# Performance work log

Measured on AMD Instinct MI355X. Metric: run time of the kernel, lower is better.

The kernel has to match this reference:

```python
import jax, jax.numpy as jnp
import numpy as np

N_NODE = 100000
N_EDGE = 1600000
D_FEAT = 64
DEPTH = 3
BASEALPHA = 1.0


def setup_inputs() -> dict:
    key = jax.random.key(0)
    k1, k2, k3 = jax.random.split(key, 3)
    x = jax.random.normal(k1, (N_NODE, D_FEAT), dtype=jnp.float32)
    edge_index = jax.random.randint(k2, (2, N_EDGE), 0, N_NODE, dtype=jnp.int64)
    edge_attr = jax.random.uniform(k3, (N_EDGE,), dtype=jnp.float32)
    # learnable polynomial coefficients, init = min(1/alpha, 1) = 1.0
    alphas = jnp.ones((DEPTH + 1,), dtype=jnp.float32)
    return {"x": x, "edge_index": edge_index, "edge_attr": edge_attr, "alphas": alphas}


def reference(x, edge_index, edge_attr, alphas):
    n = x.shape[0]
    row, col = edge_index[0], edge_index[1]
    # GCN symmetric degree normalization: val_e = d_row^-1/2 * w_e * d_col^-1/2
    deg = jax.ops.segment_sum(edge_attr, row, num_segments=n)
    safe_deg = jnp.where(deg > 0, deg, 1.0)
    dinv = jnp.where(deg > 0, jax.lax.rsqrt(safe_deg), 0.0)
    val = dinv[row] * edge_attr * dinv[col]  # [E]

    a = BASEALPHA * jnp.tanh(alphas)  # [depth+1]

    def spmm(h):  # (adj @ h): out[i] = sum_{e: row_e=i} val_e * h[col_e]
        return jax.ops.segment_sum(val[:, None] * h[col], row, num_segments=n)

    # PowerConv recurrence: x_0 = x; x_L = a_L * (adj @ x_{L-1})
    xs = [x]
    for L in range(1, DEPTH + 1):
        xs.append(a[L] * spmm(xs[-1]))
    return jnp.stack(xs, axis=1)  # [N, depth+1, d]
```

## Files before the change

kernel.cpp:

```cpp
#include <hip/hip_runtime.h>
#include <math.h>

#define N_NODE 100000
#define N_EDGE 1600000
#define D_FEAT 64
#define DEPTH  3
#define OUT_STRIDE ((DEPTH + 1) * D_FEAT)

#define NB  256
#define RPB 391
#define CAP 8192
#define S1_BS 512
#define S1_CHUNK 8192
#define S1_BLOCKS ((N_EDGE + S1_CHUNK - 1) / S1_CHUNK)

#define DEG_SCALE 33554432.0f

__device__ __forceinline__ unsigned int bf16_rne(float f) {
    unsigned int u = __float_as_uint(f);
    return (u + 0x7FFFu + ((u >> 16) & 1u)) >> 16;
}

__global__ __launch_bounds__(S1_BS) void stage1_bucket(
        const int* __restrict__ ei, const float* __restrict__ ea,
        int* __restrict__ bucket_cursor, int2* __restrict__ bucket) {
    __shared__ int hist[NB];
    __shared__ int segb[NB];
    int tid = threadIdx.x;
    int e0 = blockIdx.x * S1_CHUNK;

    for (int i = tid; i < NB; i += S1_BS) hist[i] = 0;
    __syncthreads();

    for (int k = 0; k < S1_CHUNK; k += S1_BS) {
        int e = e0 + k + tid;
        if (e < N_EDGE) {
            int r = ei[e];
            atomicAdd(&hist[r / RPB], 1);
        }
    }
    __syncthreads();

    for (int i = tid; i < NB; i += S1_BS) {
        int h = hist[i];
        segb[i] = (h > 0) ? atomicAdd(&bucket_cursor[i], h) : 0;
        hist[i] = 0;
    }
    __syncthreads();

    for (int k = 0; k < S1_CHUNK; k += S1_BS) {
        int e = e0 + k + tid;
        if (e < N_EDGE) {
            int r  = ei[e];
            int b  = r / RPB;
            int rl = r - b * RPB;
            int c  = ei[N_EDGE + e];
            float w = ea[e];
            int lofs = atomicAdd(&hist[b], 1);
            int pos  = segb[b] + lofs;
            if (pos < CAP)
                bucket[(size_t)b * CAP + pos] =
                    make_int2((rl << 17) | c, __float_as_int(w));
        }
    }
}

__global__ void bucket_scan_kernel(const int* __restrict__ bucket_cursor,
                                   int* __restrict__ bucket_base,
                                   const float* __restrict__ alphas,
                                   float* __restrict__ a_vals) {
    __shared__ int sc[NB];
    int tid = threadIdx.x;
    int v = bucket_cursor[tid];
    sc[tid] = v;
    __syncthreads();
    for (int off = 1; off < NB; off <<= 1) {
        int t = (tid >= off) ? sc[tid - off] : 0;
        __syncthreads();
        sc[tid] += t;
        __syncthreads();
    }
    bucket_base[tid] = sc[tid] - v;
    if (tid < DEPTH + 1) a_vals[tid] = tanhf(alphas[tid]);
}

__global__ __launch_bounds__(1024) void stage2a_rows(
        const int2* __restrict__ bucket, const int* __restrict__ bucket_cnt,
        const int* __restrict__ bucket_base,
        int* __restrict__ row_ptr, int* __restrict__ row_end,
        float* __restrict__ dinv) {
    __shared__ int          rcnt[RPB];
    __shared__ unsigned int wdeg[RPB];
    __shared__ int          sc[512];
    int b = blockIdx.x, tid = threadIdx.x;

    for (int i = tid; i < RPB; i += 1024) { rcnt[i] = 0; wdeg[i] = 0u; }
    __syncthreads();

    int cnt = bucket_cnt[b];
    const int2* src = bucket + (size_t)b * CAP;
    for (int i = tid; i < cnt; i += 1024) {
        int2 e = src[i];
        int rl = e.x >> 17;
        float w = __int_as_float(e.y);
        atomicAdd(&rcnt[rl], 1);
        atomicAdd(&wdeg[rl], (unsigned int)(w * DEG_SCALE + 0.5f));
    }
    __syncthreads();

    int v = 0;
    if (tid < 512) {
        v = (tid < RPB) ? rcnt[tid] : 0;
        sc[tid] = v;
    }
    __syncthreads();
    for (int off = 1; off < 512; off <<= 1) {
        int t = 0;
        if (tid < 512 && tid >= off) t = sc[tid - off];
        __syncthreads();
        if (tid < 512) sc[tid] += t;
        __syncthreads();
    }

    if (tid < RPB) {
        int row = b * RPB + tid;
        if (row < N_NODE) {
            int base = bucket_base[b] + sc[tid] - v;
            row_ptr[row] = base;
            row_end[row] = base + rcnt[tid];
            float d = (float)wdeg[tid] * (1.0f / DEG_SCALE);
            dinv[row] = (d > 0.0f) ? rsqrtf(d) : 0.0f;
        }
    }
}

__global__ __launch_bounds__(1024) void stage2b_place(
        const int2* __restrict__ bucket, const int* __restrict__ bucket_cnt,
        const int* __restrict__ bucket_base, const int* __restrict__ row_ptr,
        const float* __restrict__ dinv, int2* __restrict__ csr) {
    __shared__ int   lcur[RPB];
    __shared__ float dinv_l[RPB];
    __shared__ int2  staged[CAP];
    int b = blockIdx.x, tid = threadIdx.x;
    int base_b = bucket_base[b];
    int row0 = b * RPB;

    for (int i = tid; i < RPB; i += 1024) {
        int row = row0 + i;
        if (row < N_NODE) {
            lcur[i]   = row_ptr[row] - base_b;
            dinv_l[i] = dinv[row];
        } else {
            lcur[i] = 0; dinv_l[i] = 0.0f;
        }
    }
    __syncthreads();

    int cnt = bucket_cnt[b];
    const int2* src = bucket + (size_t)b * CAP;
    for (int i = tid; i < cnt; i += 1024) {
        int2 e = src[i];
        int rl = e.x >> 17;
        int c  = e.x & 0x1FFFF;
        float w = __int_as_float(e.y);
        int pos = atomicAdd(&lcur[rl], 1);
        float val = dinv_l[rl] * w * dinv[c];
        staged[pos] = make_int2(c, __float_as_int(val));
    }
    __syncthreads();

    for (int i = tid; i < cnt; i += 1024) csr[base_b + i] = staged[i];
}

__global__ void init_out_kernel(const float* __restrict__ x,
                                float* __restrict__ out,
                                unsigned short* __restrict__ hb0,
                                int write_hb) {
    int i = blockIdx.x * blockDim.x + threadIdx.x;
    if (i < N_NODE * D_FEAT) {
        int n = i >> 6;
        int d = i & 63;
        float v = x[i];
        out[(size_t)n * OUT_STRIDE + d] = v;
        if (write_hb) hb0[i] = (unsigned short)bf16_rne(v);
    }
}

__global__ void spmm_bf16_kernel(const int* __restrict__ row_ptr,
                                 const int* __restrict__ row_end,
                                 const int2* __restrict__ csr,
                                 const float* __restrict__ a_vals,
                                 const unsigned short* __restrict__ hsrc,
                                 unsigned short* __restrict__ hdst,
                                 float* __restrict__ out,
                                 int L, int write_hdst) {
    int node = blockIdx.x * (blockDim.x >> 6) + (threadIdx.x >> 6);
    int lane = threadIdx.x & 63;
    if (node >= N_NODE) return;
    int beg = row_ptr[node];
    int end = row_end[node];
    int g = lane >> 4;
    int q = lane & 15;

    float4 acc = make_float4(0.0f, 0.0f, 0.0f, 0.0f);

    for (int chunk = beg; chunk < end; chunk += 64) {
        int idx = chunk + lane;
        int2 pv = (idx < end) ? csr[idx] : make_int2(0, 0);
        int navail = end - chunk;
        if (navail > 64) navail = 64;
        for (int t = 0; t < navail; t += 4) {
            int sub = t + g;
            int   cc = __shfl(pv.x, sub);
            float vv = __int_as_float(__shfl(pv.y, sub));
            bool valid = (sub < navail);
            int   c_safe = valid ? cc : 0;
            float v_safe = valid ? vv : 0.0f;
            uint2 hv = *(const uint2*)&hsrc[(size_t)c_safe * D_FEAT + (q << 2)];
            float h0 = __uint_as_float((hv.x & 0xFFFFu) << 16);
            float h1 = __uint_as_float(hv.x & 0xFFFF0000u);
            float h2 = __uint_as_float((hv.y & 0xFFFFu) << 16);
            float h3 = __uint_as_float(hv.y & 0xFFFF0000u);
            acc.x += v_safe * h0;
            acc.y += v_safe * h1;
            acc.z += v_safe * h2;
            acc.w += v_safe * h3;
        }
    }

    acc.x += __shfl_down(acc.x, 32);
    acc.y += __shfl_down(acc.y, 32);
    acc.z += __shfl_down(acc.z, 32);
    acc.w += __shfl_down(acc.w, 32);
    acc.x += __shfl_down(acc.x, 16);
    acc.y += __shfl_down(acc.y, 16);
    acc.z += __shfl_down(acc.z, 16);
    acc.w += __shfl_down(acc.w, 16);

    if (g == 0) {
        float aL = a_vals[L];
        float4 r = make_float4(aL * acc.x, aL * acc.y, aL * acc.z, aL * acc.w);
        *(float4*)&out[(size_t)node * OUT_STRIDE + L * D_FEAT + (q << 2)] = r;
        if (write_hdst) {
            uint2 o;
            o.x = bf16_rne(r.x) | (bf16_rne(r.y) << 16);
            o.y = bf16_rne(r.z) | (bf16_rne(r.w) << 16);
            *(uint2*)&hdst[(size_t)node * D_FEAT + (q << 2)] = o;
        }
    }
}

__global__ void spmm_f32_kernel(const int* __restrict__ row_ptr,
                                const int* __restrict__ row_end,
                                const int2* __restrict__ csr,
                                const float* __restrict__ a_vals,
                                float* __restrict__ out,
                                int L) {
    int node = blockIdx.x * (blockDim.x >> 6) + (threadIdx.x >> 6);
    int lane = threadIdx.x & 63;
    if (node >= N_NODE) return;
    int beg = row_ptr[node];
    int end = row_end[node];
    int g = lane >> 4;
    int q = lane & 15;
    int src_base = (L - 1) * D_FEAT + (q << 2);

    float4 acc = make_float4(0.0f, 0.0f, 0.0f, 0.0f);
    for (int chunk = beg; chunk < end; chunk += 64) {
        int idx = chunk + lane;
        int2 pv = (idx < end) ? csr[idx] : make_int2(0, 0);
        int navail = end - chunk;
        if (navail > 64) navail = 64;
        for (int t = 0; t < navail; t += 4) {
            int sub = t + g;
            int   cc = __shfl(pv.x, sub);
            float vv = __int_as_float(__shfl(pv.y, sub));
            bool valid = (sub < navail);
            int   c_safe = valid ? cc : 0;
            float v_safe = valid ? vv : 0.0f;
            const float4 hv =
                *(const float4*)&out[(size_t)c_safe * OUT_STRIDE + src_base];
            acc.x += v_safe * hv.x;
            acc.y += v_safe * hv.y;
            acc.z += v_safe * hv.z;
            acc.w += v_safe * hv.w;
        }
    }
    acc.x += __shfl_down(acc.x, 32);
    acc.y += __shfl_down(acc.y, 32);
    acc.z += __shfl_down(acc.z, 32);
    acc.w += __shfl_down(acc.w, 32);
    acc.x += __shfl_down(acc.x, 16);
    acc.y += __shfl_down(acc.y, 16);
    acc.z += __shfl_down(acc.z, 16);
    acc.w += __shfl_down(acc.w, 16);
    if (g == 0) {
        float aL = a_vals[L];
        float4 r = make_float4(aL * acc.x, aL * acc.y, aL * acc.z, aL * acc.w);
        *(float4*)&out[(size_t)node * OUT_STRIDE + L * D_FEAT + (q << 2)] = r;
    }
}

extern "C" void kernel_launch(void* const* d_in, const int* in_sizes, int n_in,
                              void* d_out, int out_size, void* d_ws, size_t ws_size,
                              hipStream_t stream) {
    const float* x      = (const float*)d_in[0];
    const int*   ei     = (const int*)d_in[1];
    const float* ea     = (const float*)d_in[2];
    const float* alphas = (const float*)d_in[3];
    float*       out    = (float*)d_out;

    int2*  csr          = (int2*)d_ws;
    int*   row_ptr      = (int*)(csr + N_EDGE);
    int*   row_end      = row_ptr + N_NODE;
    float* dinv         = (float*)(row_end + N_NODE);
    int*   bucket_cursor= (int*)(dinv + N_NODE);
    int*   bucket_base  = bucket_cursor + NB;
    float* a_vals       = (float*)(bucket_base + NB);
    int2*  bucket       = (int2*)(a_vals + 4);
    unsigned short* hb0 = (unsigned short*)bucket;
    unsigned short* hb1 = hb0 + (size_t)N_NODE * D_FEAT;

    size_t base_bytes = (size_t)((char*)bucket - (char*)d_ws);
    size_t need_bf16  = base_bytes +
        2 * (size_t)N_NODE * D_FEAT * sizeof(unsigned short);
    int use_bf16 = (ws_size >= need_bf16) ? 1 : 0;

    hipMemsetAsync(bucket_cursor, 0, NB * sizeof(int), stream);

    stage1_bucket<<<S1_BLOCKS, S1_BS, 0, stream>>>(ei, ea, bucket_cursor, bucket);
    bucket_scan_kernel<<<1, NB, 0, stream>>>(bucket_cursor, bucket_base,
                                             alphas, a_vals);
    stage2a_rows<<<NB, 1024, 0, stream>>>(bucket, bucket_cursor, bucket_base,
                                          row_ptr, row_end, dinv);
    stage2b_place<<<NB, 1024, 0, stream>>>(bucket, bucket_cursor, bucket_base,
                                           row_ptr, dinv, csr);
    init_out_kernel<<<(N_NODE * D_FEAT + 255) / 256, 256, 0, stream>>>(
        x, out, hb0, use_bf16);

    int nodes_per_block = 256 / 64;
    int spmm_blocks = (N_NODE + nodes_per_block - 1) / nodes_per_block;
    if (use_bf16) {
        spmm_bf16_kernel<<<spmm_blocks, 256, 0, stream>>>(row_ptr, row_end, csr,
                                                          a_vals, hb0, hb1, out, 1, 1);
        spmm_bf16_kernel<<<spmm_blocks, 256, 0, stream>>>(row_ptr, row_end, csr,
                                                          a_vals, hb1, hb0, out, 2, 1);
        spmm_bf16_kernel<<<spmm_blocks, 256, 0, stream>>>(row_ptr, row_end, csr,
                                                          a_vals, hb0, hb1, out, 3, 0);
    } else {
        for (int L = 1; L <= DEPTH; ++L) {
            spmm_f32_kernel<<<spmm_blocks, 256, 0, stream>>>(row_ptr, row_end, csr,
                                                             a_vals, out, L);
        }
    }
}
```

Baseline: 347.0 us.

## Fuse CSR build stages and fold degree normalization into node-side scaling

Merges the row-count/scan kernel and the placement kernel into one, so the bucket is read once and the per-edge dinv[col] gather is gone. The CSR now stores raw edge weights. The symmetric normalization moves onto the nodes: features are pre-scaled by dinv when written as bf16, and each output row is scaled by dinv on output. The bf16 SpMM now gives each lane 8 features with 16-byte loads and processes 8 edges per step, and init_out is vectorized to float4. The bf16 rounding now applies to dinv-scaled values, and the fp32 fallback gathers dinv per edge inside the SpMM loop.

```diff
diff --git a/kernel.cpp b/kernel.cpp
--- a/kernel.cpp
+++ b/kernel.cpp
@@ -84,14 +84,16 @@
     if (tid < DEPTH + 1) a_vals[tid] = tanhf(alphas[tid]);
 }
 
-__global__ __launch_bounds__(1024) void stage2a_rows(
+__global__ __launch_bounds__(1024) void stage2_fused(
         const int2* __restrict__ bucket, const int* __restrict__ bucket_cnt,
         const int* __restrict__ bucket_base,
         int* __restrict__ row_ptr, int* __restrict__ row_end,
-        float* __restrict__ dinv) {
+        float* __restrict__ dinv, int2* __restrict__ csr) {
     __shared__ int          rcnt[RPB];
     __shared__ unsigned int wdeg[RPB];
     __shared__ int          sc[512];
+    __shared__ int          lcur[RPB];
+    __shared__ int2         staged[CAP];
     int b = blockIdx.x, tid = threadIdx.x;
 
     for (int i = tid; i < RPB; i += 1024) { rcnt[i] = 0; wdeg[i] = 0u; }
@@ -109,10 +111,7 @@
     __syncthreads();
 
     int v = 0;
-    if (tid < 512) {
-        v = (tid < RPB) ? rcnt[tid] : 0;
-        sc[tid] = v;
-    }
+    if (tid < 512) { v = (tid < RPB) ? rcnt[tid] : 0; sc[tid] = v; }
     __syncthreads();
     for (int off = 1; off < 512; off <<= 1) {
         int t = 0;
@@ -122,50 +121,26 @@
         __syncthreads();
     }
 
+    int base_b = bucket_base[b];
     if (tid < RPB) {
+        int excl = sc[tid] - v;
+        lcur[tid] = excl;
         int row = b * RPB + tid;
         if (row < N_NODE) {
-            int base = bucket_base[b] + sc[tid] - v;
-            row_ptr[row] = base;
-            row_end[row] = base + rcnt[tid];
+            row_ptr[row] = base_b + excl;
+            row_end[row] = base_b + excl + rcnt[tid];
             float d = (float)wdeg[tid] * (1.0f / DEG_SCALE);
             dinv[row] = (d > 0.0f) ? rsqrtf(d) : 0.0f;
         }
     }
-}
-
-__global__ __launch_bounds__(1024) void stage2b_place(
-        const int2* __restrict__ bucket, const int* __restrict__ bucket_cnt,
-        const int* __restrict__ bucket_base, const int* __restrict__ row_ptr,
-        const float* __restrict__ dinv, int2* __restrict__ csr) {
-    __shared__ int   lcur[RPB];
-    __shared__ float dinv_l[RPB];
-    __shared__ int2  staged[CAP];
-    int b = blockIdx.x, tid = threadIdx.x;
-    int base_b = bucket_base[b];
-    int row0 = b * RPB;
-
-    for (int i = tid; i < RPB; i += 1024) {
-        int row = row0 + i;
-        if (row < N_NODE) {
-            lcur[i]   = row_ptr[row] - base_b;
-            dinv_l[i] = dinv[row];
-        } else {
-            lcur[i] = 0; dinv_l[i] = 0.0f;
-        }
-    }
-    __syncthreads();
-
-    int cnt = bucket_cnt[b];
-    const int2* src = bucket + (size_t)b * CAP;
+    __syncthreads();
+
     for (int i = tid; i < cnt; i += 1024) {
         int2 e = src[i];
         int rl = e.x >> 17;
         int c  = e.x & 0x1FFFF;
-        float w = __int_as_float(e.y);
         int pos = atomicAdd(&lcur[rl], 1);
-        float val = dinv_l[rl] * w * dinv[c];
-        staged[pos] = make_int2(c, __float_as_int(val));
+        staged[pos] = make_int2(c, e.y);
     }
     __syncthreads();
 
@@ -173,16 +148,23 @@
 }
 
 __global__ void init_out_kernel(const float* __restrict__ x,
+                                const float* __restrict__ dinv,
                                 float* __restrict__ out,
                                 unsigned short* __restrict__ hb0,
                                 int write_hb) {
     int i = blockIdx.x * blockDim.x + threadIdx.x;
-    if (i < N_NODE * D_FEAT) {
-        int n = i >> 6;
-        int d = i & 63;
-        float v = x[i];
-        out[(size_t)n * OUT_STRIDE + d] = v;
-        if (write_hb) hb0[i] = (unsigned short)bf16_rne(v);
+    if (i < N_NODE * (D_FEAT / 4)) {
+        int n  = i >> 4;
+        int d4 = (i & 15) << 2;
+        float4 v = *(const float4*)&x[(size_t)n * D_FEAT + d4];
+        *(float4*)&out[(size_t)n * OUT_STRIDE + d4] = v;
+        if (write_hb) {
+            float s = dinv[n];
+            uint2 o;
+            o.x = bf16_rne(v.x * s) | (bf16_rne(v.y * s) << 16);
+            o.y = bf16_rne(v.z * s) | (bf16_rne(v.w * s) << 16);
+            *(uint2*)&hb0[(size_t)n * D_FEAT + d4] = o;
+        }
     }
 }
 
@@ -190,6 +172,7 @@
                                  const int* __restrict__ row_end,
                                  const int2* __restrict__ csr,
                                  const float* __restrict__ a_vals,
+                                 const float* __restrict__ dinv,
                                  const unsigned short* __restrict__ hsrc,
                                  unsigned short* __restrict__ hdst,
                                  float* __restrict__ out,
@@ -199,53 +182,61 @@
     if (node >= N_NODE) return;
     int beg = row_ptr[node];
     int end = row_end[node];
-    int g = lane >> 4;
-    int q = lane & 15;
-
-    float4 acc = make_float4(0.0f, 0.0f, 0.0f, 0.0f);
+    int g = lane >> 3;
+    int q = lane & 7;
+
+    float acc[8] = {0, 0, 0, 0, 0, 0, 0, 0};
 
     for (int chunk = beg; chunk < end; chunk += 64) {
         int idx = chunk + lane;
         int2 pv = (idx < end) ? csr[idx] : make_int2(0, 0);
         int navail = end - chunk;
         if (navail > 64) navail = 64;
-        for (int t = 0; t < navail; t += 4) {
+        for (int t = 0; t < navail; t += 8) {
             int sub = t + g;
             int   cc = __shfl(pv.x, sub);
             float vv = __int_as_float(__shfl(pv.y, sub));
             bool valid = (sub < navail);
             int   c_safe = valid ? cc : 0;
             float v_safe = valid ? vv : 0.0f;
-            uint2 hv = *(const uint2*)&hsrc[(size_t)c_safe * D_FEAT + (q << 2)];
-            float h0 = __uint_as_float((hv.x & 0xFFFFu) << 16);
-            float h1 = __uint_as_float(hv.x & 0xFFFF0000u);
-            float h2 = __uint_as_float((hv.y & 0xFFFFu) << 16);
-            float h3 = __uint_as_float(hv.y & 0xFFFF0000u);
-            acc.x += v_safe * h0;
-            acc.y += v_safe * h1;
-            acc.z += v_safe * h2;
-            acc.w += v_safe * h3;
-        }
-    }
-
-    acc.x += __shfl_down(acc.x, 32);
-    acc.y += __shfl_down(acc.y, 32);
-    acc.z += __shfl_down(acc.z, 32);
-    acc.w += __shfl_down(acc.w, 32);
-    acc.x += __shfl_down(acc.x, 16);
-    acc.y += __shfl_down(acc.y, 16);
-    acc.z += __shfl_down(acc.z, 16);
-    acc.w += __shfl_down(acc.w, 16);
+            uint4 hv = *(const uint4*)&hsrc[(size_t)c_safe * D_FEAT + (q << 3)];
+            acc[0] += v_safe * __uint_as_float((hv.x & 0xFFFFu) << 16);
+            acc[1] += v_safe * __uint_as_float(hv.x & 0xFFFF0000u);
+            acc[2] += v_safe * __uint_as_float((hv.y & 0xFFFFu) << 16);
+            acc[3] += v_safe * __uint_as_float(hv.y & 0xFFFF0000u);
+            acc[4] += v_safe * __uint_as_float((hv.z & 0xFFFFu) << 16);
+            acc[5] += v_safe * __uint_as_float(hv.z & 0xFFFF0000u);
+            acc[6] += v_safe * __uint_as_float((hv.w & 0xFFFFu) << 16);
+            acc[7] += v_safe * __uint_as_float(hv.w & 0xFFFF0000u);
+        }
+    }
+
+    #pragma unroll
+    for (int j = 0; j < 8; ++j) {
+        acc[j] += __shfl_down(acc[j], 32);
+        acc[j] += __shfl_down(acc[j], 16);
+        acc[j] += __shfl_down(acc[j], 8);
+    }
 
     if (g == 0) {
+        float di = dinv[node];
         float aL = a_vals[L];
-        float4 r = make_float4(aL * acc.x, aL * acc.y, aL * acc.z, aL * acc.w);
-        *(float4*)&out[(size_t)node * OUT_STRIDE + L * D_FEAT + (q << 2)] = r;
+        float s1 = aL * di;
+        float s2 = s1 * di;
+        float4 r0 = make_float4(s1 * acc[0], s1 * acc[1],
+                                s1 * acc[2], s1 * acc[3]);
+        float4 r1 = make_float4(s1 * acc[4], s1 * acc[5],
+                                s1 * acc[6], s1 * acc[7]);
+        size_t ob = (size_t)node * OUT_STRIDE + L * D_FEAT + (q << 3);
+        *(float4*)&out[ob]     = r0;
+        *(float4*)&out[ob + 4] = r1;
         if (write_hdst) {
-            uint2 o;
-            o.x = bf16_rne(r.x) | (bf16_rne(r.y) << 16);
-            o.y = bf16_rne(r.z) | (bf16_rne(r.w) << 16);
-            *(uint2*)&hdst[(size_t)node * D_FEAT + (q << 2)] = o;
+            uint4 o;
+            o.x = bf16_rne(s2 * acc[0]) | (bf16_rne(s2 * acc[1]) << 16);
+            o.y = bf16_rne(s2 * acc[2]) | (bf16_rne(s2 * acc[3]) << 16);
+            o.z = bf16_rne(s2 * acc[4]) | (bf16_rne(s2 * acc[5]) << 16);
+            o.w = bf16_rne(s2 * acc[6]) | (bf16_rne(s2 * acc[7]) << 16);
+            *(uint4*)&hdst[(size_t)node * D_FEAT + (q << 3)] = o;
         }
     }
 }
@@ -254,6 +245,7 @@
                                 const int* __restrict__ row_end,
                                 const int2* __restrict__ csr,
                                 const float* __restrict__ a_vals,
+                                const float* __restrict__ dinv,
                                 float* __restrict__ out,
                                 int L) {
     int node = blockIdx.x * (blockDim.x >> 6) + (threadIdx.x >> 6);
@@ -277,7 +269,7 @@
             float vv = __int_as_float(__shfl(pv.y, sub));
             bool valid = (sub < navail);
             int   c_safe = valid ? cc : 0;
-            float v_safe = valid ? vv : 0.0f;
+            float v_safe = valid ? (vv * dinv[c_safe]) : 0.0f;
             const float4 hv =
                 *(const float4*)&out[(size_t)c_safe * OUT_STRIDE + src_base];
             acc.x += v_safe * hv.x;
@@ -295,8 +287,8 @@
     acc.z += __shfl_down(acc.z, 16);
     acc.w += __shfl_down(acc.w, 16);
     if (g == 0) {
-        float aL = a_vals[L];
-        float4 r = make_float4(aL * acc.x, aL * acc.y, aL * acc.z, aL * acc.w);
+        float s1 = a_vals[L] * dinv[node];
+        float4 r = make_float4(s1 * acc.x, s1 * acc.y, s1 * acc.z, s1 * acc.w);
         *(float4*)&out[(size_t)node * OUT_STRIDE + L * D_FEAT + (q << 2)] = r;
     }
 }
@@ -331,26 +323,24 @@
     stage1_bucket<<<S1_BLOCKS, S1_BS, 0, stream>>>(ei, ea, bucket_cursor, bucket);
     bucket_scan_kernel<<<1, NB, 0, stream>>>(bucket_cursor, bucket_base,
                                              alphas, a_vals);
-    stage2a_rows<<<NB, 1024, 0, stream>>>(bucket, bucket_cursor, bucket_base,
-                                          row_ptr, row_end, dinv);
-    stage2b_place<<<NB, 1024, 0, stream>>>(bucket, bucket_cursor, bucket_base,
-                                           row_ptr, dinv, csr);
-    init_out_kernel<<<(N_NODE * D_FEAT + 255) / 256, 256, 0, stream>>>(
-        x, out, hb0, use_bf16);
+    stage2_fused<<<NB, 1024, 0, stream>>>(bucket, bucket_cursor, bucket_base,
+                                          row_ptr, row_end, dinv, csr);
+    init_out_kernel<<<(N_NODE * (D_FEAT / 4) + 255) / 256, 256, 0, stream>>>(
+        x, dinv, out, hb0, use_bf16);
 
     int nodes_per_block = 256 / 64;
     int spmm_blocks = (N_NODE + nodes_per_block - 1) / nodes_per_block;
     if (use_bf16) {
         spmm_bf16_kernel<<<spmm_blocks, 256, 0, stream>>>(row_ptr, row_end, csr,
-                                                          a_vals, hb0, hb1, out, 1, 1);
+            a_vals, dinv, hb0, hb1, out, 1, 1);
         spmm_bf16_kernel<<<spmm_blocks, 256, 0, stream>>>(row_ptr, row_end, csr,
-                                                          a_vals, hb1, hb0, out, 2, 1);
+            a_vals, dinv, hb1, hb0, out, 2, 1);
         spmm_bf16_kernel<<<spmm_blocks, 256, 0, stream>>>(row_ptr, row_end, csr,
-                                                          a_vals, hb0, hb1, out, 3, 0);
+            a_vals, dinv, hb0, hb1, out, 3, 0);
     } else {
         for (int L = 1; L <= DEPTH; ++L) {
             spmm_f32_kernel<<<spmm_blocks, 256, 0, stream>>>(row_ptr, row_end, csr,
-                                                             a_vals, out, L);
-        }
-    }
-}
+                a_vals, dinv, out, L);
+        }
+    }
+}
```

After: 331.2 us. 1.05x faster.
